# Performance work log

Measured on AMD Instinct MI355X. Metric: run time of the kernel, lower is better.

The kernel has to match this reference:

```python
import jax, jax.numpy as jnp
import numpy as np

N_NODES = 100000
N_EDGES = 1600000
D_IN = 128
D_HID = 128
D_OUT = 128


def setup_inputs() -> dict:
    key = jax.random.key(0)
    ks = jax.random.split(key, 8)
    x = jax.random.normal(ks[0], (N_NODES, D_IN), dtype=jnp.float32)
    edge_index = jax.random.randint(ks[1], (2, N_EDGES), 0, N_NODES, dtype=jnp.int64)
    # GraphConv layer 1: lin_rel (with bias) applied to aggregated messages, lin_root (no bias) to x
    s1 = 1.0 / np.sqrt(D_IN)
    W1_rel = jax.random.uniform(ks[2], (D_IN, D_HID), jnp.float32, -s1, s1)
    b1 = jax.random.uniform(ks[3], (D_HID,), jnp.float32, -s1, s1)
    W1_root = jax.random.uniform(ks[4], (D_IN, D_HID), jnp.float32, -s1, s1)
    s2 = 1.0 / np.sqrt(D_HID)
    W2_rel = jax.random.uniform(ks[5], (D_HID, D_OUT), jnp.float32, -s2, s2)
    b2 = jax.random.uniform(ks[6], (D_OUT,), jnp.float32, -s2, s2)
    W2_root = jax.random.uniform(ks[7], (D_HID, D_OUT), jnp.float32, -s2, s2)
    return {"x": x, "edge_index": edge_index, "W1_rel": W1_rel, "b1": b1,
            "W1_root": W1_root, "W2_rel": W2_rel, "b2": b2, "W2_root": W2_root}


def graph_conv(x, src, dst, W_rel, b, W_root, n_nodes):
    # PyG GraphConv (aggr='add'): out_i = W_rel @ sum_{j->i} x_j + b + W_root @ x_i
    msgs = jnp.take(x, src, axis=0)                       # [E, F] gather
    agg = jax.ops.segment_sum(msgs, dst, num_segments=n_nodes)  # [N, F] scatter-add
    return agg @ W_rel + b + x @ W_root


def reference(x, edge_index, W1_rel, b1, W1_root, W2_rel, b2, W2_root):
    src, dst = edge_index[0], edge_index[1]
    n = x.shape[0]
    h = graph_conv(x, src, dst, W1_rel, b1, W1_root, n)
    h = jax.nn.relu(h)
    out = graph_conv(h, src, dst, W2_rel, b2, W2_root, n)
    return out
```

## Files before the change

### kernel.cpp

```cpp
#include <hip/hip_runtime.h>

#define D 128
#define TILE_R 32
#define LDS_STRIDE 260
#define GBM 64
#define APAD 264

#define NB 512
#define NPB 256
#define EPB_A 2048

typedef __attribute__((ext_vector_type(8))) short bf16x8;
typedef __attribute__((ext_vector_type(4))) float f32x4;

static __device__ __forceinline__ ushort f2b(float f) {
    union { float f; uint u; } v; v.f = f;
    uint r = (v.u + 0x7FFFu + ((v.u >> 16) & 1u)) >> 16;
    return (ushort)r;
}
static __device__ __forceinline__ float blo(uint u) {
    union { uint u; float f; } v; v.u = u << 16; return v.f;
}
static __device__ __forceinline__ float bhi(uint u) {
    union { uint u; float f; } v; v.u = u & 0xFFFF0000u; return v.f;
}

__global__ __launch_bounds__(256) void prep_kernel(
    const float* __restrict__ x, ushort* __restrict__ xb, int n8,
    const float* __restrict__ W1rel, const float* __restrict__ W1root, ushort* __restrict__ Wt1,
    const float* __restrict__ W2rel, const float* __restrict__ W2root, ushort* __restrict__ Wt2,
    const int* __restrict__ dst, int* __restrict__ bcnt, int nedges,
    int nConvBlocks, int nCountBlocks)
{
    __shared__ int h[NB];
    const int b = blockIdx.x, t = threadIdx.x;

    if (b < nConvBlocks) {
        int i = b * 256 + t;
        if (i >= n8) return;
        float4 a = reinterpret_cast<const float4*>(x)[i * 2];
        float4 c = reinterpret_cast<const float4*>(x)[i * 2 + 1];
        uint4 r;
        r.x = f2b(a.x) | ((uint)f2b(a.y) << 16);
        r.y = f2b(a.z) | ((uint)f2b(a.w) << 16);
        r.z = f2b(c.x) | ((uint)f2b(c.y) << 16);
        r.w = f2b(c.z) | ((uint)f2b(c.w) << 16);
        reinterpret_cast<uint4*>(xb)[i] = r;
    } else if (b < nConvBlocks + 256) {
        int wb = b - nConvBlocks;
        const float* Wrel  = (wb < 128) ? W1rel  : W2rel;
        const float* Wroot = (wb < 128) ? W1root : W2root;
        ushort* Wt = (wb < 128) ? Wt1 : Wt2;
        int idx = (wb & 127) * 256 + t;
        int n = idx >> 8, k = idx & 255;
        float v = (k < 128) ? Wrel[(size_t)k * D + n] : Wroot[(size_t)(k - 128) * D + n];
        Wt[idx] = f2b(v);
    } else {
        int cb = b - nConvBlocks - 256;
        if (cb >= nCountBlocks) return;
        for (int i = t; i < NB; i += 256) h[i] = 0;
        __syncthreads();
        int base = cb * EPB_A;
        #pragma unroll
        for (int i = 0; i < 8; ++i) {
            int e = base + i * 256 + t;
            if (e < nedges) atomicAdd(&h[dst[e] >> 8], 1);
        }
        __syncthreads();
        for (int i = t; i < NB; i += 256) if (h[i]) atomicAdd(&bcnt[i], h[i]);
    }
}


__global__ __launch_bounds__(512) void bucket_scan_kernel(
    const int* __restrict__ bcnt, int* __restrict__ bbase, int* __restrict__ bcur)
{
    __shared__ int sh[NB];
    int t = threadIdx.x;
    int v = bcnt[t];
    sh[t] = v; __syncthreads();
    int val = v;
    for (int off = 1; off < NB; off <<= 1) {
        int u = (t >= off) ? sh[t - off] : 0;
        __syncthreads();
        val += u; sh[t] = val; __syncthreads();
    }
    int excl = val - v;
    bbase[t] = excl;
    bcur[t] = excl;
}

__global__ __launch_bounds__(256) void bucket_scatter_kernel(
    const int* __restrict__ src, const int* __restrict__ dst,
    int* __restrict__ bcur, uint* __restrict__ ebuf, int nedges)
{
    __shared__ int h[NB];
    __shared__ int res[NB];
    int t = threadIdx.x;
    for (int i = t; i < NB; i += 256) h[i] = 0;
    __syncthreads();
    int base = blockIdx.x * EPB_A;
    int d[8], s[8], bkt[8];
    #pragma unroll
    for (int i = 0; i < 8; ++i) {
        int e = base + i * 256 + t;
        if (e < nedges) {
            d[i] = dst[e]; s[i] = src[e]; bkt[i] = d[i] >> 8;
            atomicAdd(&h[bkt[i]], 1);
        } else bkt[i] = -1;
    }
    __syncthreads();
    for (int i = t; i < NB; i += 256) {
        int c = h[i];
        res[i] = c ? atomicAdd(&bcur[i], c) : 0;
    }
    __syncthreads();
    #pragma unroll
    for (int i = 0; i < 8; ++i) {
        if (bkt[i] >= 0) {
            int pos = atomicAdd(&res[bkt[i]], 1);
            ebuf[pos] = ((uint)(d[i] & (NPB - 1)) << 17) | (uint)s[i];
        }
    }
}

__global__ __launch_bounds__(256) void csr_finalize_kernel(
    const uint* __restrict__ ebuf, const int* __restrict__ bbase,
    const int* __restrict__ bcnt, int* __restrict__ csr_src,
    int* __restrict__ ends, int n)
{
    __shared__ int cnt[NPB];
    __shared__ int cur[NPB];
    __shared__ int sh[NPB];
    int b = blockIdx.x, t = threadIdx.x;
    int ebase = bbase[b];
    int ecnt = bcnt[b];
    cnt[t] = 0;
    __syncthreads();
    for (int i = t; i < ecnt; i += 256)
        atomicAdd(&cnt[ebuf[ebase + i] >> 17], 1);
    __syncthreads();
    int v = cnt[t];
    sh[t] = v; __syncthreads();
    int val = v;
    for (int off = 1; off < 256; off <<= 1) {
        int u = (t >= off) ? sh[t - off] : 0;
        __syncthreads();
        val += u; sh[t] = val; __syncthreads();
    }
    int node = b * NPB + t;
    if (node < n) ends[node] = ebase + val;
    cur[t] = ebase + (val - v);
    __syncthreads();
    for (int i = t; i < ecnt; i += 256) {
        uint p = ebuf[ebase + i];
        int pos = atomicAdd(&cur[p >> 17], 1);
        csr_src[pos] = (int)(p & 0x1FFFFu);
    }
}

__global__ __launch_bounds__(256, 4) void layer_fused_kernel(
    const ushort* __restrict__ feat, const int* __restrict__ csr_src,
    const int* __restrict__ ends, const ushort* __restrict__ Wt,
    const float* __restrict__ bias, float* outf, ushort* outb,
    int n, int mode)
{
    __shared__ ushort As[GBM * APAD];
    const int t = threadIdx.x;
    const int wave = t >> 6, lane = t & 63;
    const int base = blockIdx.x * GBM;
    const int l15 = lane & 15;

    #pragma unroll
    for (int m = 0; m < 4; ++m) {
        int q = t + m * 256;
        int r = q >> 4, c = q & 15;
        int row = base + r;
        uint4 v = make_uint4(0, 0, 0, 0);
        if (row < n) v = reinterpret_cast<const uint4*>(feat + (size_t)row * D)[c];
        *reinterpret_cast<uint4*>(&As[r * APAD + 128 + c * 8]) = v;
    }

    {
        const int g = t >> 4, l = t & 15;
        #pragma unroll 1
        for (int sub = 0; sub < 4; ++sub) {
            int r = g * 4 + sub;
            int node = base + r;
            float a0=0,a1=0,a2=0,a3=0,a4=0,a5=0,a6=0,a7=0;
            float c0=0,c1=0,c2=0,c3=0,c4=0,c5=0,c6=0,c7=0;
            float e0=0,e1=0,e2=0,e3=0,e4=0,e5=0,e6=0,e7=0;
            float g0=0,g1=0,g2=0,g3=0,g4=0,g5=0,g6=0,g7=0;
            if (node < n) {
                int jb = (node == 0) ? 0 : ends[node - 1];
                int je = ends[node];
                int j = jb;
                for (; j + 4 <= je; j += 4) {
                    int s0 = csr_src[j], s1 = csr_src[j + 1];
                    int s2 = csr_src[j + 2], s3 = csr_src[j + 3];
                    uint4 v0 = reinterpret_cast<const uint4*>(feat + (size_t)s0 * D)[l];
                    uint4 v1 = reinterpret_cast<const uint4*>(feat + (size_t)s1 * D)[l];
                    uint4 v2 = reinterpret_cast<const uint4*>(feat + (size_t)s2 * D)[l];
                    uint4 v3 = reinterpret_cast<const uint4*>(feat + (size_t)s3 * D)[l];
                    a0 += blo(v0.x); a1 += bhi(v0.x); a2 += blo(v0.y); a3 += bhi(v0.y);
                    a4 += blo(v0.z); a5 += bhi(v0.z); a6 += blo(v0.w); a7 += bhi(v0.w);
                    c0 += blo(v1.x); c1 += bhi(v1.x); c2 += blo(v1.y); c3 += bhi(v1.y);
                    c4 += blo(v1.z); c5 += bhi(v1.z); c6 += blo(v1.w); c7 += bhi(v1.w);
                    e0 += blo(v2.x); e1 += bhi(v2.x); e2 += blo(v2.y); e3 += bhi(v2.y);
                    e4 += blo(v2.z); e5 += bhi(v2.z); e6 += blo(v2.w); e7 += bhi(v2.w);
                    g0 += blo(v3.x); g1 += bhi(v3.x); g2 += blo(v3.y); g3 += bhi(v3.y);
                    g4 += blo(v3.z); g5 += bhi(v3.z); g6 += blo(v3.w); g7 += bhi(v3.w);
                }
                for (; j < je; ++j) {
                    int s0 = csr_src[j];
                    uint4 v0 = reinterpret_cast<const uint4*>(feat + (size_t)s0 * D)[l];
                    a0 += blo(v0.x); a1 += bhi(v0.x); a2 += blo(v0.y); a3 += bhi(v0.y);
                    a4 += blo(v0.z); a5 += bhi(v0.z); a6 += blo(v0.w); a7 += bhi(v0.w);
                }
            }
            uint4 rp;
            rp.x = f2b(a0 + c0 + e0 + g0) | ((uint)f2b(a1 + c1 + e1 + g1) << 16);
            rp.y = f2b(a2 + c2 + e2 + g2) | ((uint)f2b(a3 + c3 + e3 + g3) << 16);
            rp.z = f2b(a4 + c4 + e4 + g4) | ((uint)f2b(a5 + c5 + e5 + g5) << 16);
            rp.w = f2b(a6 + c6 + e6 + g6) | ((uint)f2b(a7 + c7 + e7 + g7) << 16);
            *reinterpret_cast<uint4*>(&As[r * APAD + l * 8]) = rp;
        }
    }
    __syncthreads();

    const int bcol0 = wave * 32;
    f32x4 acc[4][2];
    #pragma unroll
    for (int rt = 0; rt < 4; ++rt)
        #pragma unroll
        for (int nt = 0; nt < 2; ++nt) acc[rt][nt] = (f32x4){0.f, 0.f, 0.f, 0.f};

    #pragma unroll 1
    for (int ks = 0; ks < 8; ++ks) {
        const int kk = ks * 32 + (lane >> 4) * 8;
        bf16x8 a0_ = *reinterpret_cast<const bf16x8*>(&As[(l15 +  0) * APAD + kk]);
        bf16x8 a1_ = *reinterpret_cast<const bf16x8*>(&As[(l15 + 16) * APAD + kk]);
        bf16x8 a2_ = *reinterpret_cast<const bf16x8*>(&As[(l15 + 32) * APAD + kk]);
        bf16x8 a3_ = *reinterpret_cast<const bf16x8*>(&As[(l15 + 48) * APAD + kk]);
        bf16x8 b0_ = *reinterpret_cast<const bf16x8*>(Wt + (size_t)(bcol0 + l15) * 256 + kk);
        bf16x8 b1_ = *reinterpret_cast<const bf16x8*>(Wt + (size_t)(bcol0 + 16 + l15) * 256 + kk);
        acc[0][0] = __builtin_amdgcn_mfma_f32_16x16x32_bf16(a0_, b0_, acc[0][0], 0, 0, 0);
        acc[0][1] = __builtin_amdgcn_mfma_f32_16x16x32_bf16(a0_, b1_, acc[0][1], 0, 0, 0);
        acc[1][0] = __builtin_amdgcn_mfma_f32_16x16x32_bf16(a1_, b0_, acc[1][0], 0, 0, 0);
        acc[1][1] = __builtin_amdgcn_mfma_f32_16x16x32_bf16(a1_, b1_, acc[1][1], 0, 0, 0);
        acc[2][0] = __builtin_amdgcn_mfma_f32_16x16x32_bf16(a2_, b0_, acc[2][0], 0, 0, 0);
        acc[2][1] = __builtin_amdgcn_mfma_f32_16x16x32_bf16(a2_, b1_, acc[2][1], 0, 0, 0);
        acc[3][0] = __builtin_amdgcn_mfma_f32_16x16x32_bf16(a3_, b0_, acc[3][0], 0, 0, 0);
        acc[3][1] = __builtin_amdgcn_mfma_f32_16x16x32_bf16(a3_, b1_, acc[3][1], 0, 0, 0);
    }

    #pragma unroll
    for (int rt = 0; rt < 4; ++rt)
        #pragma unroll
        for (int nt = 0; nt < 2; ++nt) {
            int col = bcol0 + nt * 16 + l15;
            float bv = bias[col];
            #pragma unroll
            for (int r = 0; r < 4; ++r) {
                int row = base + rt * 16 + (lane >> 4) * 4 + r;
                if (row >= n) continue;
                float v = acc[rt][nt][r] + bv;
                if (mode == 0) {
                    v = fmaxf(v, 0.f);
                    outb[(size_t)row * D + col] = f2b(v);
                } else {
                    outf[(size_t)row * D + col] = v;
                }
            }
        }
}


__global__ __launch_bounds__(256) void scatter_add_kernel(
    const float* __restrict__ feat, const int* __restrict__ src,
    const int* __restrict__ dst, float* agg, int nedges)
{
    int tid = blockIdx.x * 256 + threadIdx.x;
    int e = tid >> 5;
    if (e >= nedges) return;
    int l = tid & 31;
    int s = src[e];
    int d = dst[e];
    const float4 v = *reinterpret_cast<const float4*>(feat + (size_t)s * D + l * 4);
    float* o = agg + (size_t)d * D + l * 4;
    unsafeAtomicAdd(o + 0, v.x);
    unsafeAtomicAdd(o + 1, v.y);
    unsafeAtomicAdd(o + 2, v.z);
    unsafeAtomicAdd(o + 3, v.w);
}

__global__ __launch_bounds__(256) void gemm_fused_kernel(
    const float* __restrict__ A1, const float* A2,
    const float* __restrict__ Wrel, const float* __restrict__ Wroot,
    const float* __restrict__ bias, float* out, int n, int do_relu)
{
    __shared__ float Asf[TILE_R * LDS_STRIDE];
    const int t = threadIdx.x;
    const int base = blockIdx.x * TILE_R;

    #pragma unroll
    for (int m = 0; m < 8; ++m) {
        int q = t + m * 256;
        int r = q >> 6;
        int kk = (q & 63) << 2;
        int row = base + r;
        float4 v = make_float4(0.f, 0.f, 0.f, 0.f);
        if (row < n) {
            const float* p = (kk < 128) ? (A1 + (size_t)row * D + kk)
                                        : (A2 + (size_t)row * D + (kk - 128));
            v = *reinterpret_cast<const float4*>(p);
        }
        *reinterpret_cast<float4*>(&Asf[r * LDS_STRIDE + kk]) = v;
    }
    __syncthreads();

    const int rg = t >> 5;
    const int c0 = (t & 31) << 2;

    float acc[4][4];
    #pragma unroll
    for (int i = 0; i < 4; ++i)
        #pragma unroll
        for (int j = 0; j < 4; ++j) acc[i][j] = 0.f;

    const float* Wmats[2] = {Wrel, Wroot};
    #pragma unroll
    for (int half = 0; half < 2; ++half) {
        const float* W = Wmats[half];
        const int kb = half * 128;
        for (int k = 0; k < 128; k += 4) {
            float w[4][4];
            #pragma unroll
            for (int kk = 0; kk < 4; ++kk) {
                float4 wv = *reinterpret_cast<const float4*>(W + (size_t)(k + kk) * D + c0);
                w[kk][0] = wv.x; w[kk][1] = wv.y; w[kk][2] = wv.z; w[kk][3] = wv.w;
            }
            #pragma unroll
            for (int i = 0; i < 4; ++i) {
                float4 av = *reinterpret_cast<const float4*>(&Asf[(rg * 4 + i) * LDS_STRIDE + kb + k]);
                float a[4] = {av.x, av.y, av.z, av.w};
                #pragma unroll
                for (int kk = 0; kk < 4; ++kk)
                    #pragma unroll
                    for (int j = 0; j < 4; ++j)
                        acc[i][j] = fmaf(a[kk], w[kk][j], acc[i][j]);
            }
        }
    }

    float4 bv = *reinterpret_cast<const float4*>(bias + c0);
    float b[4] = {bv.x, bv.y, bv.z, bv.w};
    #pragma unroll
    for (int i = 0; i < 4; ++i) {
        int row = base + rg * 4 + i;
        if (row >= n) continue;
        float o[4];
        #pragma unroll
        for (int j = 0; j < 4; ++j) {
            float v = acc[i][j] + b[j];
            if (do_relu) v = fmaxf(v, 0.f);
            o[j] = v;
        }
        *reinterpret_cast<float4*>(out + (size_t)row * D + c0) =
            make_float4(o[0], o[1], o[2], o[3]);
    }
}

extern "C" void kernel_launch(void* const* d_in, const int* in_sizes, int n_in,
                              void* d_out, int out_size, void* d_ws, size_t ws_size,
                              hipStream_t stream) {
    const float* x       = (const float*)d_in[0];
    const int*   ei      = (const int*)d_in[1];
    const float* W1_rel  = (const float*)d_in[2];
    const float* b1      = (const float*)d_in[3];
    const float* W1_root = (const float*)d_in[4];
    const float* W2_rel  = (const float*)d_in[5];
    const float* b2      = (const float*)d_in[6];
    const float* W2_root = (const float*)d_in[7];
    float* out = (float*)d_out;

    const int E = in_sizes[1] / 2;
    const int N = in_sizes[0] / D;
    const int* src = ei;
    const int* dst = ei + E;

    size_t hbB   = ((size_t)N * D * 2 + 255) & ~(size_t)255;
    size_t xbB   = ((size_t)N * D * 2 + 255) & ~(size_t)255;
    size_t csrB  = ((size_t)E * 4 + 255) & ~(size_t)255;
    size_t endB  = ((size_t)(N + 1) * 4 + 255) & ~(size_t)255;
    size_t bktB  = ((size_t)(3 * NB + 8) * 4 + 255) & ~(size_t)255;
    size_t wtB   = (size_t)128 * 256 * 2;
    size_t need = hbB + xbB + csrB + endB + bktB + 2 * wtB;

    bool pack_ok = (N <= 131072) && ((size_t)E * 4 <= hbB);

    if (ws_size >= need && pack_ok) {
        char* w = (char*)d_ws;
        ushort* hb      = (ushort*)w;            w += hbB;
        ushort* xb      = (ushort*)w;            w += xbB;
        int*    csr_src = (int*)w;               w += csrB;
        int*    ends    = (int*)w;               w += endB;
        int*    bcnt    = (int*)w;
        int*    bbase   = bcnt + NB;
        int*    bcur    = bbase + NB;            w += bktB;
        ushort* Wt1     = (ushort*)w;            w += wtB;
        ushort* Wt2     = (ushort*)w;
        uint*   ebuf    = (uint*)hb;

        const int aBlocks = (E + EPB_A - 1) / EPB_A;
        const int nbu = (N + NPB - 1) / NPB;
        const int n8 = N * D / 8;
        const int nConvBlocks = (n8 + 255) / 256;

        hipMemsetAsync(bcnt, 0, NB * sizeof(int), stream);
        prep_kernel<<<nConvBlocks + 256 + aBlocks, 256, 0, stream>>>(
            x, xb, n8, W1_rel, W1_root, Wt1, W2_rel, W2_root, Wt2,
            dst, bcnt, E, nConvBlocks, aBlocks);

        bucket_scan_kernel<<<1, NB, 0, stream>>>(bcnt, bbase, bcur);
        bucket_scatter_kernel<<<aBlocks, 256, 0, stream>>>(src, dst, bcur, ebuf, E);
        csr_finalize_kernel<<<nbu, 256, 0, stream>>>(ebuf, bbase, bcnt, csr_src, ends, N);

        int layerBlocks = (N + GBM - 1) / GBM;

        layer_fused_kernel<<<layerBlocks, 256, 0, stream>>>(
            xb, csr_src, ends, Wt1, b1, nullptr, hb, N, 0);
        layer_fused_kernel<<<layerBlocks, 256, 0, stream>>>(
            hb, csr_src, ends, Wt2, b2, out, nullptr, N, 1);
    } else {
        float* agg = (float*)d_ws;
        size_t aggBytes = (size_t)N * D * sizeof(float);
        int scatterBlocks = (E * 32 + 255) / 256;
        int gemmBlocks = (N + TILE_R - 1) / TILE_R;
        hipMemsetAsync(agg, 0, aggBytes, stream);
        scatter_add_kernel<<<scatterBlocks, 256, 0, stream>>>(x, src, dst, agg, E);
        gemm_fused_kernel<<<gemmBlocks, 256, 0, stream>>>(agg, x, W1_rel, W1_root, b1, out, N, 1);
        hipMemsetAsync(agg, 0, aggBytes, stream);
        scatter_add_kernel<<<scatterBlocks, 256, 0, stream>>>(out, src, dst, agg, E);
        gemm_fused_kernel<<<gemmBlocks, 256, 0, stream>>>(agg, out, W2_rel, W2_root, b2, out, N, 0);
    }
}
```

Baseline: 262.5 us.

## Balance aggregation with LDS work counter and prefetch weight fragments into registers

Replaces the fixed assignment of four nodes per 16-lane group with dynamic row stealing through a shared-memory atomic counter, so groups whose nodes have short neighbor lists pick up more rows. The gather loop is unrolled to eight neighbors with a single accumulator set, which puts more loads in flight but lengthens the dependent add chain. Weight fragments for the MFMA stage are loaded into registers before aggregation so their latency overlaps the gather. The extra 64 VGPRs of prefetched B fragments may lower occupancy under the launch bound of four blocks.

```diff
diff --git a/kernel.cpp b/kernel.cpp
--- a/kernel.cpp
+++ b/kernel.cpp
@@ -166,10 +166,14 @@
     int n, int mode)
 {
     __shared__ ushort As[GBM * APAD];
+    __shared__ int ctr;
     const int t = threadIdx.x;
     const int wave = t >> 6, lane = t & 63;
     const int base = blockIdx.x * GBM;
     const int l15 = lane & 15;
+    const int bcol0 = wave * 32;
+
+    if (t == 0) ctr = 0;
 
     #pragma unroll
     for (int m = 0; m < 4; ++m) {
@@ -181,35 +185,58 @@
         *reinterpret_cast<uint4*>(&As[r * APAD + 128 + c * 8]) = v;
     }
 
+    bf16x8 Bfrag[2][8];
+    #pragma unroll
+    for (int ks = 0; ks < 8; ++ks) {
+        const int kk = ks * 32 + (lane >> 4) * 8;
+        Bfrag[0][ks] = *reinterpret_cast<const bf16x8*>(Wt + (size_t)(bcol0 + l15) * 256 + kk);
+        Bfrag[1][ks] = *reinterpret_cast<const bf16x8*>(Wt + (size_t)(bcol0 + 16 + l15) * 256 + kk);
+    }
+
+    __syncthreads();
+
     {
-        const int g = t >> 4, l = t & 15;
-        #pragma unroll 1
-        for (int sub = 0; sub < 4; ++sub) {
-            int r = g * 4 + sub;
-            int node = base + r;
+        const int l = t & 15;
+        for (;;) {
+            int my;
+            if (l == 0) my = atomicAdd(&ctr, 1);
+            my = __shfl(my, lane & 48, 64);
+            if (my >= GBM) break;
+            int node = base + my;
             float a0=0,a1=0,a2=0,a3=0,a4=0,a5=0,a6=0,a7=0;
-            float c0=0,c1=0,c2=0,c3=0,c4=0,c5=0,c6=0,c7=0;
-            float e0=0,e1=0,e2=0,e3=0,e4=0,e5=0,e6=0,e7=0;
-            float g0=0,g1=0,g2=0,g3=0,g4=0,g5=0,g6=0,g7=0;
             if (node < n) {
                 int jb = (node == 0) ? 0 : ends[node - 1];
                 int je = ends[node];
                 int j = jb;
-                for (; j + 4 <= je; j += 4) {
-                    int s0 = csr_src[j], s1 = csr_src[j + 1];
+                for (; j + 8 <= je; j += 8) {
+                    int s0 = csr_src[j + 0], s1 = csr_src[j + 1];
                     int s2 = csr_src[j + 2], s3 = csr_src[j + 3];
+                    int s4 = csr_src[j + 4], s5 = csr_src[j + 5];
+                    int s6 = csr_src[j + 6], s7 = csr_src[j + 7];
                     uint4 v0 = reinterpret_cast<const uint4*>(feat + (size_t)s0 * D)[l];
                     uint4 v1 = reinterpret_cast<const uint4*>(feat + (size_t)s1 * D)[l];
                     uint4 v2 = reinterpret_cast<const uint4*>(feat + (size_t)s2 * D)[l];
                     uint4 v3 = reinterpret_cast<const uint4*>(feat + (size_t)s3 * D)[l];
+                    uint4 v4 = reinterpret_cast<const uint4*>(feat + (size_t)s4 * D)[l];
+                    uint4 v5 = reinterpret_cast<const uint4*>(feat + (size_t)s5 * D)[l];
+                    uint4 v6 = reinterpret_cast<const uint4*>(feat + (size_t)s6 * D)[l];
+                    uint4 v7 = reinterpret_cast<const uint4*>(feat + (size_t)s7 * D)[l];
                     a0 += blo(v0.x); a1 += bhi(v0.x); a2 += blo(v0.y); a3 += bhi(v0.y);
                     a4 += blo(v0.z); a5 += bhi(v0.z); a6 += blo(v0.w); a7 += bhi(v0.w);
-                    c0 += blo(v1.x); c1 += bhi(v1.x); c2 += blo(v1.y); c3 += bhi(v1.y);
-                    c4 += blo(v1.z); c5 += bhi(v1.z); c6 += blo(v1.w); c7 += bhi(v1.w);
-                    e0 += blo(v2.x); e1 += bhi(v2.x); e2 += blo(v2.y); e3 += bhi(v2.y);
-                    e4 += blo(v2.z); e5 += bhi(v2.z); e6 += blo(v2.w); e7 += bhi(v2.w);
-                    g0 += blo(v3.x); g1 += bhi(v3.x); g2 += blo(v3.y); g3 += bhi(v3.y);
-                    g4 += blo(v3.z); g5 += bhi(v3.z); g6 += blo(v3.w); g7 += bhi(v3.w);
+                    a0 += blo(v1.x); a1 += bhi(v1.x); a2 += blo(v1.y); a3 += bhi(v1.y);
+                    a4 += blo(v1.z); a5 += bhi(v1.z); a6 += blo(v1.w); a7 += bhi(v1.w);
+                    a0 += blo(v2.x); a1 += bhi(v2.x); a2 += blo(v2.y); a3 += bhi(v2.y);
+                    a4 += blo(v2.z); a5 += bhi(v2.z); a6 += blo(v2.w); a7 += bhi(v2.w);
+                    a0 += blo(v3.x); a1 += bhi(v3.x); a2 += blo(v3.y); a3 += bhi(v3.y);
+                    a4 += blo(v3.z); a5 += bhi(v3.z); a6 += blo(v3.w); a7 += bhi(v3.w);
+                    a0 += blo(v4.x); a1 += bhi(v4.x); a2 += blo(v4.y); a3 += bhi(v4.y);
+                    a4 += blo(v4.z); a5 += bhi(v4.z); a6 += blo(v4.w); a7 += bhi(v4.w);
+                    a0 += blo(v5.x); a1 += bhi(v5.x); a2 += blo(v5.y); a3 += bhi(v5.y);
+                    a4 += blo(v5.z); a5 += bhi(v5.z); a6 += blo(v5.w); a7 += bhi(v5.w);
+                    a0 += blo(v6.x); a1 += bhi(v6.x); a2 += blo(v6.y); a3 += bhi(v6.y);
+                    a4 += blo(v6.z); a5 += bhi(v6.z); a6 += blo(v6.w); a7 += bhi(v6.w);
+                    a0 += blo(v7.x); a1 += bhi(v7.x); a2 += blo(v7.y); a3 += bhi(v7.y);
+                    a4 += blo(v7.z); a5 += bhi(v7.z); a6 += blo(v7.w); a7 += bhi(v7.w);
                 }
                 for (; j < je; ++j) {
                     int s0 = csr_src[j];
@@ -219,16 +246,15 @@
                 }
             }
             uint4 rp;
-            rp.x = f2b(a0 + c0 + e0 + g0) | ((uint)f2b(a1 + c1 + e1 + g1) << 16);
-            rp.y = f2b(a2 + c2 + e2 + g2) | ((uint)f2b(a3 + c3 + e3 + g3) << 16);
-            rp.z = f2b(a4 + c4 + e4 + g4) | ((uint)f2b(a5 + c5 + e5 + g5) << 16);
-            rp.w = f2b(a6 + c6 + e6 + g6) | ((uint)f2b(a7 + c7 + e7 + g7) << 16);
-            *reinterpret_cast<uint4*>(&As[r * APAD + l * 8]) = rp;
-        }
-    }
-    __syncthreads();
-
-    const int bcol0 = wave * 32;
+            rp.x = f2b(a0) | ((uint)f2b(a1) << 16);
+            rp.y = f2b(a2) | ((uint)f2b(a3) << 16);
+            rp.z = f2b(a4) | ((uint)f2b(a5) << 16);
+            rp.w = f2b(a6) | ((uint)f2b(a7) << 16);
+            *reinterpret_cast<uint4*>(&As[my * APAD + l * 8]) = rp;
+        }
+    }
+    __syncthreads();
+
     f32x4 acc[4][2];
     #pragma unroll
     for (int rt = 0; rt < 4; ++rt)
@@ -242,16 +268,14 @@
         bf16x8 a1_ = *reinterpret_cast<const bf16x8*>(&As[(l15 + 16) * APAD + kk]);
         bf16x8 a2_ = *reinterpret_cast<const bf16x8*>(&As[(l15 + 32) * APAD + kk]);
         bf16x8 a3_ = *reinterpret_cast<const bf16x8*>(&As[(l15 + 48) * APAD + kk]);
-        bf16x8 b0_ = *reinterpret_cast<const bf16x8*>(Wt + (size_t)(bcol0 + l15) * 256 + kk);
-        bf16x8 b1_ = *reinterpret_cast<const bf16x8*>(Wt + (size_t)(bcol0 + 16 + l15) * 256 + kk);
-        acc[0][0] = __builtin_amdgcn_mfma_f32_16x16x32_bf16(a0_, b0_, acc[0][0], 0, 0, 0);
-        acc[0][1] = __builtin_amdgcn_mfma_f32_16x16x32_bf16(a0_, b1_, acc[0][1], 0, 0, 0);
-        acc[1][0] = __builtin_amdgcn_mfma_f32_16x16x32_bf16(a1_, b0_, acc[1][0], 0, 0, 0);
-        acc[1][1] = __builtin_amdgcn_mfma_f32_16x16x32_bf16(a1_, b1_, acc[1][1], 0, 0, 0);
-        acc[2][0] = __builtin_amdgcn_mfma_f32_16x16x32_bf16(a2_, b0_, acc[2][0], 0, 0, 0);
-        acc[2][1] = __builtin_amdgcn_mfma_f32_16x16x32_bf16(a2_, b1_, acc[2][1], 0, 0, 0);
-        acc[3][0] = __builtin_amdgcn_mfma_f32_16x16x32_bf16(a3_, b0_, acc[3][0], 0, 0, 0);
-        acc[3][1] = __builtin_amdgcn_mfma_f32_16x16x32_bf16(a3_, b1_, acc[3][1], 0, 0, 0);
+        acc[0][0] = __builtin_amdgcn_mfma_f32_16x16x32_bf16(a0_, Bfrag[0][ks], acc[0][0], 0, 0, 0);
+        acc[0][1] = __builtin_amdgcn_mfma_f32_16x16x32_bf16(a0_, Bfrag[1][ks], acc[0][1], 0, 0, 0);
+        acc[1][0] = __builtin_amdgcn_mfma_f32_16x16x32_bf16(a1_, Bfrag[0][ks], acc[1][0], 0, 0, 0);
+        acc[1][1] = __builtin_amdgcn_mfma_f32_16x16x32_bf16(a1_, Bfrag[1][ks], acc[1][1], 0, 0, 0);
+        acc[2][0] = __builtin_amdgcn_mfma_f32_16x16x32_bf16(a2_, Bfrag[0][ks], acc[2][0], 0, 0, 0);
+        acc[2][1] = __builtin_amdgcn_mfma_f32_16x16x32_bf16(a2_, Bfrag[1][ks], acc[2][1], 0, 0, 0);
+        acc[3][0] = __builtin_amdgcn_mfma_f32_16x16x32_bf16(a3_, Bfrag[0][ks], acc[3][0], 0, 0, 0);
+        acc[3][1] = __builtin_amdgcn_mfma_f32_16x16x32_bf16(a3_, Bfrag[1][ks], acc[3][1], 0, 0, 0);
     }
 
     #pragma unroll
```

Result: slower. 315.4 us (+20.1%).
